# Kernel tuning notes

Measured on AMD Instinct MI355X. Metric: run time of the kernel, lower is better.

## Reference

```python
import jax, jax.numpy as jnp
import numpy as np

K = 9        # kernel_size
DIL = 6      # dilation
SIGMA = 1.0  # gaussian bandwidth
BN_EPS = 1e-5


def setup_inputs() -> dict:
    key = jax.random.key(0)
    ks = jax.random.split(key, 6)
    B, Cin, Cout, N = 8, 256, 256, 8192
    x = jax.random.normal(ks[0], (B, Cin, N), jnp.float32)
    coords = jax.random.normal(ks[1], (B, 3, N), jnp.float32)
    rotations = jax.random.normal(ks[2], (B, 3, N), jnp.float32)
    distances = jax.random.uniform(ks[3], (B, N), jnp.float32)
    W = jax.random.normal(ks[4], (Cout, Cin, K), jnp.float32) * 0.02
    bias = jnp.zeros((Cout,), jnp.float32)
    gamma = jnp.ones((Cout,), jnp.float32)
    beta = jnp.zeros((Cout,), jnp.float32)
    return dict(x=x, coords=coords, rotations=rotations, distances=distances,
                W=W, bias=bias, gamma=gamma, beta=beta)


def _tap_weight(c0, cj, r0, rj, d0, dj, sigma):
    # Gaussian weight from 3D coordinate offset + curve-distance offset,
    # modulated by rotation alignment |cos(r_i, r_j)|.
    dc = jnp.sum((c0 - cj) ** 2, axis=1)          # [B,N]
    dd = (d0 - dj) ** 2                            # [B,N]
    g = jnp.exp(-(dc + dd) / (2.0 * sigma * sigma))
    num = jnp.sum(r0 * rj, axis=1)
    den = jnp.sqrt(jnp.sum(r0 * r0, axis=1) * jnp.sum(rj * rj, axis=1)) + 1e-8
    return g * jnp.abs(num / den)                  # [B,N]


def reference(x, coords, rotations, distances, W, bias, gamma, beta):
    B, Cin, N = x.shape
    Cout = W.shape[0]
    pad = DIL * (K // 2)  # same-length output for the dilated conv
    pw3 = ((0, 0), (0, 0), (pad, pad))
    xp = jnp.pad(x, pw3)
    cp = jnp.pad(coords, pw3)
    rp = jnp.pad(rotations, pw3)
    dp = jnp.pad(distances, ((0, 0), (pad, pad)))

    out = jnp.zeros((B, Cout, N), x.dtype)
    for k in range(K):  # fixed, small tap loop
        off = k * DIL
        xk = jax.lax.dynamic_slice_in_dim(xp, off, N, axis=2)
        ck = jax.lax.dynamic_slice_in_dim(cp, off, N, axis=2)
        rk = jax.lax.dynamic_slice_in_dim(rp, off, N, axis=2)
        dk = jax.lax.dynamic_slice_in_dim(dp, off, N, axis=1)
        g = _tap_weight(coords, ck, rotations, rk, distances, dk, SIGMA)  # [B,N]
        out = out + jnp.einsum('oc,bcn->bon', W[:, :, k], xk * g[:, None, :])
    out = out + bias[None, :, None]

    # BatchNorm1d (training-mode batch stats over B and N per channel)
    mean = jnp.mean(out, axis=(0, 2), keepdims=True)
    var = jnp.var(out, axis=(0, 2), keepdims=True)
    out = (out - mean) / jnp.sqrt(var + BN_EPS)
    out = out * gamma[None, :, None] + beta[None, :, None]
    return jax.nn.relu(out)
```

## Files before the change

kernel.cpp:

```cpp
#include <hip/hip_runtime.h>

#define KTAPS 9
#define DIL 6
#define BN_EPS 1e-5f
#define BB 8
#define CIN 256
#define COUT 256
#define NPTS 8192
#define BN 64
#define BSTRIDE 40

typedef __attribute__((ext_vector_type(8))) short short8;
typedef __attribute__((ext_vector_type(4))) float f32x4;

__device__ __forceinline__ unsigned short f2bf(float f) {
  union { float f; unsigned u; } v; v.f = f;
  unsigned r = v.u + 0x7fffu + ((v.u >> 16) & 1u);
  return (unsigned short)(r >> 16);
}

__global__ __launch_bounds__(256)
void pre_kernel(const float* __restrict__ W, short* __restrict__ Wa,
                float* __restrict__ sums) {
  int bid = blockIdx.x;
  if (bid < 2304) {
    int idx = bid * 256 + threadIdx.x;
    int kk = idx & 31;
    int mi = (idx >> 5) & 255;
    int chunk = idx >> 13;
    int ktap = chunk >> 3;
    int c = ((chunk & 7) << 5) + kk;
    Wa[idx] = (short)f2bf(W[(size_t)mi * (CIN * KTAPS) + c * KTAPS + ktap]);
  } else {
    if (threadIdx.x < 512) sums[threadIdx.x] = 0.f;
  }
}

__global__ __launch_bounds__(256, 2)
void conv_mfma(const float* __restrict__ x, const float* __restrict__ coords,
               const float* __restrict__ rot, const float* __restrict__ dist,
               const short* __restrict__ Wa, const float* __restrict__ bias,
               float* __restrict__ out,
               float* __restrict__ sums1, float* __restrict__ sums2) {
  __shared__ short B_all[KTAPS][BN][BSTRIDE];
  __shared__ float g_lds[KTAPS][BN];

  const int tid = threadIdx.x;
  const int b = blockIdx.y;
  const int n0 = blockIdx.x * BN;
  const int wave = tid >> 6;
  const int lane = tid & 63;
  const int col = lane & 15;
  const int quad = lane >> 4;
  const int nb = tid & 63;
  const int q8 = (tid >> 6) * 8;

  {
    const float* cb = coords + (size_t)b * 3 * NPTS;
    const float* rb = rot + (size_t)b * 3 * NPTS;
    const float* db = dist + (size_t)b * NPTS;
    int n = n0 + nb;
    float c0x = cb[n], c0y = cb[NPTS + n], c0z = cb[2 * NPTS + n];
    float r0x = rb[n], r0y = rb[NPTS + n], r0z = rb[2 * NPTS + n];
    float d0 = db[n];
    float r0n = r0x * r0x + r0y * r0y + r0z * r0z;
    for (int k = wave; k < KTAPS; k += 4) {
      int j = n + (k - KTAPS / 2) * DIL;
      float gv = 0.f;
      if (j >= 0 && j < NPTS) {
        float dcx = c0x - cb[j], dcy = c0y - cb[NPTS + j], dcz = c0z - cb[2 * NPTS + j];
        float dc = dcx * dcx + dcy * dcy + dcz * dcz;
        float dd = d0 - db[j];
        dd *= dd;
        float gauss = expf(-(dc + dd) * 0.5f);
        float rjx = rb[j], rjy = rb[NPTS + j], rjz = rb[2 * NPTS + j];
        float num = r0x * rjx + r0y * rjy + r0z * rjz;
        float den = sqrtf(r0n * (rjx * rjx + rjy * rjy + rjz * rjz)) + 1e-8f;
        gv = gauss * fabsf(num / den);
      }
      g_lds[k][nb] = gv;
    }
  }
  __syncthreads();

  const float* xb = x + (size_t)b * CIN * NPTS;
  const int arow0 = (wave * 64 + col) * 32 + quad * 8;

  short8 afA[4], afB[4];
#define LOADAF(AF, CHUNK)                                               \
  {                                                                     \
    const short* p_ = Wa + (size_t)(CHUNK) * 8192 + arow0;              \
    _Pragma("unroll")                                                   \
    for (int m = 0; m < 4; ++m) AF[m] = *(const short8*)(p_ + m * 512); \
  }

#define TAPM(K, AF)                                                     \
  {                                                                     \
    _Pragma("unroll")                                                   \
    for (int j = 0; j < 4; ++j) {                                       \
      short8 bfv = *(const short8*)&B_all[K][j * 16 + col][quad * 8];   \
      _Pragma("unroll")                                                 \
      for (int m = 0; m < 4; ++m)                                       \
        acc[m][j] = __builtin_amdgcn_mfma_f32_16x16x32_bf16(AF[m], bfv, acc[m][j], 0, 0, 0); \
    }                                                                   \
  }

  f32x4 acc[4][4];
#pragma unroll
  for (int m = 0; m < 4; ++m)
#pragma unroll
    for (int j = 0; j < 4; ++j) acc[m][j] = (f32x4)0.f;

  for (int c8 = 0; c8 < 8; ++c8) {
    LOADAF(afA, c8);

    {
      const float* xc = xb + (size_t)(c8 * 32 + q8) * NPTS;
#pragma unroll 1
      for (int k = 0; k < KTAPS; ++k) {
        int jpos = n0 + nb + (k - KTAPS / 2) * DIL;
        int jc = jpos < 0 ? 0 : (jpos >= NPTS ? NPTS - 1 : jpos);
        float gk = g_lds[k][nb];
        short8 p;
#pragma unroll
        for (int cc = 0; cc < 8; ++cc)
          p[cc] = (short)f2bf(xc[(size_t)cc * NPTS + jc] * gk);
        *(short8*)&B_all[k][nb][q8] = p;
      }
    }
    __syncthreads();

    LOADAF(afB, 8 + c8);   TAPM(0, afA);
    LOADAF(afA, 16 + c8);  TAPM(1, afB);
    LOADAF(afB, 24 + c8);  TAPM(2, afA);
    LOADAF(afA, 32 + c8);  TAPM(3, afB);
    LOADAF(afB, 40 + c8);  TAPM(4, afA);
    LOADAF(afA, 48 + c8);  TAPM(5, afB);
    LOADAF(afB, 56 + c8);  TAPM(6, afA);
    LOADAF(afA, 64 + c8);  TAPM(7, afB);
    TAPM(8, afA);
    __syncthreads();
  }

  const int obase = wave * 64;
  float* outp = out + (size_t)b * COUT * NPTS + n0;
#pragma unroll
  for (int m = 0; m < 4; ++m) {
    const int o0 = obase + m * 16 + quad * 4;
    const float4 bv = *(const float4*)&bias[o0];
#pragma unroll
    for (int j = 0; j < 4; ++j) {
      acc[m][j][0] += bv.x; acc[m][j][1] += bv.y;
      acc[m][j][2] += bv.z; acc[m][j][3] += bv.w;
    }
#pragma unroll
    for (int r = 0; r < 4; ++r) {
      float s1 = 0.f, s2 = 0.f;
#pragma unroll
      for (int j = 0; j < 4; ++j) {
        float v = acc[m][j][r];
        s1 += v; s2 += v * v;
      }
      s1 += __shfl_xor(s1, 1); s2 += __shfl_xor(s2, 1);
      s1 += __shfl_xor(s1, 2); s2 += __shfl_xor(s2, 2);
      s1 += __shfl_xor(s1, 4); s2 += __shfl_xor(s2, 4);
      s1 += __shfl_xor(s1, 8); s2 += __shfl_xor(s2, 8);
      if (col == 0) {
        atomicAdd(&sums1[o0 + r], s1);
        atomicAdd(&sums2[o0 + r], s2);
      }
#pragma unroll
      for (int j = 0; j < 4; ++j)
        outp[(size_t)(o0 + r) * NPTS + j * 16 + col] = acc[m][j][r];
    }
  }
}

__global__ __launch_bounds__(256)
void bn_apply(float* __restrict__ out, const float* __restrict__ sums1,
              const float* __restrict__ sums2, const float* __restrict__ gamma,
              const float* __restrict__ beta) {
  int bo = blockIdx.x;
  int o = bo & (COUT - 1);
  const float inv = 1.f / (float)(BB * NPTS);
  float mean = sums1[o] * inv;
  float var = sums2[o] * inv - mean * mean;
  float scale = gamma[o] * rsqrtf(var + BN_EPS);
  float shift = beta[o] - mean * scale;
  float4* p = (float4*)(out + (size_t)bo * NPTS);
  for (int i = threadIdx.x; i < NPTS / 4; i += blockDim.x) {
    float4 v = p[i];
    v.x = fmaxf(fmaf(v.x, scale, shift), 0.f);
    v.y = fmaxf(fmaf(v.y, scale, shift), 0.f);
    v.z = fmaxf(fmaf(v.z, scale, shift), 0.f);
    v.w = fmaxf(fmaf(v.w, scale, shift), 0.f);
    p[i] = v;
  }
}

extern "C" void kernel_launch(void* const* d_in, const int* in_sizes, int n_in,
                              void* d_out, int out_size, void* d_ws, size_t ws_size,
                              hipStream_t stream) {
  const float* x      = (const float*)d_in[0];
  const float* coords = (const float*)d_in[1];
  const float* rot    = (const float*)d_in[2];
  const float* dist   = (const float*)d_in[3];
  const float* W      = (const float*)d_in[4];
  const float* bias   = (const float*)d_in[5];
  const float* gamma  = (const float*)d_in[6];
  const float* beta   = (const float*)d_in[7];
  float* out = (float*)d_out;

  float* ws    = (float*)d_ws;
  float* sums1 = ws;
  float* sums2 = ws + 256;
  short* Wa    = (short*)(ws + 512);

  pre_kernel<<<2305, 256, 0, stream>>>(W, Wa, sums1);
  conv_mfma<<<dim3(NPTS / BN, BB), 256, 0, stream>>>(x, coords, rot, dist, Wa, bias, out, sums1, sums2);
  bn_apply<<<BB * COUT, 256, 0, stream>>>(out, sums1, sums2, gamma, beta);
}
```

Before: 324.3 us.

## Stage x window via async global-to-LDS DMA and software-pipeline tap build with MFMA

```diff
diff --git a/kernel.cpp b/kernel.cpp
--- a/kernel.cpp
+++ b/kernel.cpp
@@ -8,6 +8,7 @@
 #define COUT 256
 #define NPTS 8192
 #define BN 64
+#define XOFF 32
 #define BSTRIDE 40
 
 typedef __attribute__((ext_vector_type(8))) short short8;
@@ -17,6 +18,12 @@
   union { float f; unsigned u; } v; v.f = f;
   unsigned r = v.u + 0x7fffu + ((v.u >> 16) & 1u);
   return (unsigned short)(r >> 16);
+}
+
+__device__ __forceinline__ void async16(const void* gp, void* lp) {
+  __builtin_amdgcn_global_load_lds(
+      (const __attribute__((address_space(1))) unsigned int*)gp,
+      (__attribute__((address_space(3))) unsigned int*)lp, 16, 0, 0);
 }
 
 __global__ __launch_bounds__(256)
@@ -36,13 +43,14 @@
   }
 }
 
-__global__ __launch_bounds__(256, 2)
+__global__ __launch_bounds__(256, 3)
 void conv_mfma(const float* __restrict__ x, const float* __restrict__ coords,
                const float* __restrict__ rot, const float* __restrict__ dist,
                const short* __restrict__ Wa, const float* __restrict__ bias,
                float* __restrict__ out,
                float* __restrict__ sums1, float* __restrict__ sums2) {
-  __shared__ short B_all[KTAPS][BN][BSTRIDE];
+  __shared__ float x_win[2][4][32][32];
+  __shared__ short B_lds[2][BN][BSTRIDE];
   __shared__ float g_lds[KTAPS][BN];
 
   const int tid = threadIdx.x;
@@ -52,14 +60,12 @@
   const int lane = tid & 63;
   const int col = lane & 15;
   const int quad = lane >> 4;
-  const int nb = tid & 63;
-  const int q8 = (tid >> 6) * 8;
 
   {
     const float* cb = coords + (size_t)b * 3 * NPTS;
     const float* rb = rot + (size_t)b * 3 * NPTS;
     const float* db = dist + (size_t)b * NPTS;
-    int n = n0 + nb;
+    const int n = n0 + lane;
     float c0x = cb[n], c0y = cb[NPTS + n], c0z = cb[2 * NPTS + n];
     float r0x = rb[n], r0y = rb[NPTS + n], r0z = rb[2 * NPTS + n];
     float d0 = db[n];
@@ -78,15 +84,16 @@
         float den = sqrtf(r0n * (rjx * rjx + rjy * rjy + rjz * rjz)) + 1e-8f;
         gv = gauss * fabsf(num / den);
       }
-      g_lds[k][nb] = gv;
+      g_lds[k][lane] = gv;
     }
   }
-  __syncthreads();
 
   const float* xb = x + (size_t)b * CIN * NPTS;
   const int arow0 = (wave * 64 + col) * 32 + quad * 8;
-
-  short8 afA[4], afB[4];
+  const int wrB = lane * BSTRIDE + ((wave ^ ((lane >> 3) & 3)) << 3);
+
+  short8 af[2][4];
+
 #define LOADAF(AF, CHUNK)                                               \
   {                                                                     \
     const short* p_ = Wa + (size_t)(CHUNK) * 8192 + arow0;              \
@@ -94,52 +101,108 @@
     for (int m = 0; m < 4; ++m) AF[m] = *(const short8*)(p_ + m * 512); \
   }
 
-#define TAPM(K, AF)                                                     \
-  {                                                                     \
+#define STAGE_DMA(C8N)                                                  \
+  {                                                                     \
+    const int buf_ = (C8N)&1;                                           \
+    const int ch_ = wave * 8 + (lane >> 3);                             \
+    const float* gr_ = xb + (size_t)((C8N)*32 + ch_) * NPTS;            \
+    const int cg_ = (lane & 7) * 4;                                     \
+    _Pragma("unroll")                                                   \
+    for (int q_ = 0; q_ < 4; ++q_) {                                    \
+      int jg_ = n0 - XOFF + q_ * 32 + cg_;                              \
+      jg_ = jg_ < 0 ? 0 : (jg_ > NPTS - 4 ? NPTS - 4 : jg_);            \
+      async16(gr_ + jg_, (float*)&x_win[buf_][q_][wave * 8][0] + lane * 4); \
+    }                                                                   \
+  }
+
+#define BUILD(K, P, XC)                                                 \
+  {                                                                     \
+    float g_ = g_lds[K][lane];                                          \
+    const int w_ = lane + ((K)-KTAPS / 2) * DIL + XOFF;                 \
+    const float* xp_ = &x_win[XC][0][0][0] + ((w_ >> 5) << 10) + (w_ & 31) + wave * 256; \
+    short8 p_;                                                          \
+    _Pragma("unroll")                                                   \
+    for (int cc = 0; cc < 8; ++cc)                                      \
+      p_[cc] = (short)f2bf(xp_[cc * 32] * g_);                          \
+    *(short8*)(&B_lds[P][0][0] + wrB) = p_;                             \
+  }
+
+#define MFMA_TAP(P, AF)                                                 \
+  {                                                                     \
+    const short* bb_ = &B_lds[P][0][0];                                 \
     _Pragma("unroll")                                                   \
     for (int j = 0; j < 4; ++j) {                                       \
-      short8 bfv = *(const short8*)&B_all[K][j * 16 + col][quad * 8];   \
+      short8 bfv_ = *(const short8*)(bb_ + (j * 16 + col) * BSTRIDE +   \
+                                     ((quad ^ ((2 * j + (col >> 3)) & 3)) << 3)); \
       _Pragma("unroll")                                                 \
       for (int m = 0; m < 4; ++m)                                       \
-        acc[m][j] = __builtin_amdgcn_mfma_f32_16x16x32_bf16(AF[m], bfv, acc[m][j], 0, 0, 0); \
+        acc[m][j] = __builtin_amdgcn_mfma_f32_16x16x32_bf16(AF[m], bfv_, acc[m][j], 0, 0, 0); \
     }                                                                   \
   }
 
+#define BAR()                                                           \
+  {                                                                     \
+    asm volatile("s_waitcnt lgkmcnt(0)" ::: "memory");                  \
+    __builtin_amdgcn_s_barrier();                                       \
+    __builtin_amdgcn_sched_barrier(0);                                  \
+  }
+
+#define BARFULL()                                                       \
+  {                                                                     \
+    asm volatile("s_waitcnt vmcnt(0) lgkmcnt(0)" ::: "memory");         \
+    __builtin_amdgcn_s_barrier();                                       \
+    __builtin_amdgcn_sched_barrier(0);                                  \
+  }
+
+#define TAPX(K, C8)                                                     \
+  {                                                                     \
+    LOADAF(af[((K) + 1 + ((C8)&1)) & 1], 8 * ((K) + 1) + (C8));         \
+    BUILD((K) + 1, ((C8) + (K) + 1) & 1, (C8)&1);                       \
+    MFMA_TAP(((C8) + (K)) & 1, af[((K) + ((C8)&1)) & 1]);               \
+    BAR();                                                              \
+  }
+
+#define C8BODY(C8, DN)                                                  \
+  {                                                                     \
+    if (DN) STAGE_DMA((C8) + 1);                                        \
+    TAPX(0, C8)                                                         \
+    TAPX(1, C8)                                                         \
+    TAPX(2, C8)                                                         \
+    TAPX(3, C8)                                                         \
+    TAPX(4, C8)                                                         \
+    TAPX(5, C8)                                                         \
+    TAPX(6, C8)                                                         \
+    TAPX(7, C8)                                                         \
+          \
+    BARFULL();                                                          \
+    if (DN) {                                                           \
+      LOADAF(af[((C8) + 1) & 1], (C8) + 1);                             \
+      BUILD(0, ((C8) + 1) & 1, ((C8) + 1) & 1);                         \
+    }                                                                   \
+    MFMA_TAP((C8)&1, af[(C8)&1]);                                       \
+    BAR();                                                              \
+  }
+
   f32x4 acc[4][4];
 #pragma unroll
   for (int m = 0; m < 4; ++m)
 #pragma unroll
     for (int j = 0; j < 4; ++j) acc[m][j] = (f32x4)0.f;
 
-  for (int c8 = 0; c8 < 8; ++c8) {
-    LOADAF(afA, c8);
-
-    {
-      const float* xc = xb + (size_t)(c8 * 32 + q8) * NPTS;
+  STAGE_DMA(0);
+  LOADAF(af[0], 0);
+  asm volatile("s_waitcnt vmcnt(0)" ::: "memory");
+  __syncthreads();
+  BUILD(0, 0, 0);
+  __syncthreads();
+
 #pragma unroll 1
-      for (int k = 0; k < KTAPS; ++k) {
-        int jpos = n0 + nb + (k - KTAPS / 2) * DIL;
-        int jc = jpos < 0 ? 0 : (jpos >= NPTS ? NPTS - 1 : jpos);
-        float gk = g_lds[k][nb];
-        short8 p;
-#pragma unroll
-        for (int cc = 0; cc < 8; ++cc)
-          p[cc] = (short)f2bf(xc[(size_t)cc * NPTS + jc] * gk);
-        *(short8*)&B_all[k][nb][q8] = p;
-      }
-    }
-    __syncthreads();
-
-    LOADAF(afB, 8 + c8);   TAPM(0, afA);
-    LOADAF(afA, 16 + c8);  TAPM(1, afB);
-    LOADAF(afB, 24 + c8);  TAPM(2, afA);
-    LOADAF(afA, 32 + c8);  TAPM(3, afB);
-    LOADAF(afB, 40 + c8);  TAPM(4, afA);
-    LOADAF(afA, 48 + c8);  TAPM(5, afB);
-    LOADAF(afB, 56 + c8);  TAPM(6, afA);
-    LOADAF(afA, 64 + c8);  TAPM(7, afB);
-    TAPM(8, afA);
-    __syncthreads();
+  for (int c2 = 0; c2 < 4; ++c2) {
+    const int c8a = 2 * c2;
+    const int c8b = 2 * c2 + 1;
+    const bool dnb = (c2 < 3);
+    C8BODY(c8a, true);
+    C8BODY(c8b, dnb);
   }
 
   const int obase = wave * 64;
```

New measurement: 313.0 us. 3.5% less time.
